# Optimization experiments

Hardware: AMD Instinct MI355X
Metric: run time of the kernel (lower is better)

## Reference

```python
import jax, jax.numpy as jnp
import numpy as np

B, T, C, H = 4, 2048, 1024, 16
D = C // H  # head_dim = 64


def setup_inputs() -> dict:
    key = jax.random.key(0)
    ks = jax.random.split(key, 5)
    scale = 0.02
    return {
        "x": jax.random.normal(ks[0], (B, T, C), dtype=jnp.float32),
        "w_qkv": jax.random.normal(ks[1], (C, 3 * C), dtype=jnp.float32) * scale,
        "b_qkv": jnp.zeros((3 * C,), dtype=jnp.float32),
        "w_out": jax.random.normal(ks[2], (C, C), dtype=jnp.float32) * scale,
        "b_out": jnp.zeros((C,), dtype=jnp.float32),
    }


def reference(x, w_qkv, b_qkv, w_out, b_out):
    Bx, Tx, Cx = x.shape
    qkv = x @ w_qkv + b_qkv  # [B,T,3C]
    q, k, v = jnp.split(qkv, 3, axis=-1)
    # [B,T,C] -> [B,H,T,D]
    def heads(t):
        return t.reshape(Bx, Tx, H, D).transpose(0, 2, 1, 3)
    q, k, v = heads(q), heads(k), heads(v)
    scores = jnp.einsum("bhtd,bhsd->bhts", q, k) / jnp.sqrt(jnp.float32(D))
    causal = jnp.tril(jnp.ones((Tx, Tx), dtype=bool))
    scores = jnp.where(causal[None, None], scores, -jnp.inf)
    attn = jax.nn.softmax(scores, axis=-1)
    y = jnp.einsum("bhts,bhsd->bhtd", attn, v)  # [B,H,T,D]
    y = y.transpose(0, 2, 1, 3).reshape(Bx, Tx, Cx)
    return y @ w_out + b_out
```

## Files before the change

### kernel.cpp

```cpp
#include <hip/hip_runtime.h>
#include <hip/hip_bf16.h>
#include <math.h>

typedef __bf16 bf16;
typedef __bf16 bf16x8 __attribute__((ext_vector_type(8)));
typedef __bf16 bf16x4 __attribute__((ext_vector_type(4)));
typedef float  f32x4  __attribute__((ext_vector_type(4)));

__device__ __forceinline__ void gld_lds16(const bf16* g, bf16* l) {
    void* gv = (void*)g;
    __builtin_amdgcn_global_load_lds(
        (__attribute__((address_space(1))) void*)gv,
        (__attribute__((address_space(3))) void*)l, 16, 0, 0);
}

__global__ void k_cvt_bf16(const float* __restrict__ in, bf16* __restrict__ out, int n4) {
    int i = blockIdx.x * blockDim.x + threadIdx.x;
    if (i < n4) {
        float4 v = ((const float4*)in)[i];
        bf16x4 o;
        o[0] = (bf16)v.x; o[1] = (bf16)v.y; o[2] = (bf16)v.z; o[3] = (bf16)v.w;
        ((bf16x4*)out)[i] = o;
    }
}

__global__ void k_transpose_cvt(const float* __restrict__ in, bf16* __restrict__ out,
                                int R, int C) {
    __shared__ float tile[64][68];
    int c0 = blockIdx.x * 64, r0 = blockIdx.y * 64;
    int tid = threadIdx.x;
#pragma unroll
    for (int i = 0; i < 4; ++i) {
        int chunk = tid + i * 256;
        int r = chunk >> 4, c4 = (chunk & 15) * 4;
        float4 v = *(const float4*)(in + (size_t)(r0 + r) * C + c0 + c4);
        tile[r][c4 + 0] = v.x; tile[r][c4 + 1] = v.y;
        tile[r][c4 + 2] = v.z; tile[r][c4 + 3] = v.w;
    }
    __syncthreads();
#pragma unroll
    for (int i = 0; i < 2; ++i) {
        int chunk = tid + i * 256;
        int c = chunk >> 3, k8 = (chunk & 7) * 8;
        bf16x8 v;
#pragma unroll
        for (int j = 0; j < 8; ++j) v[j] = (bf16)tile[k8 + j][c];
        *(bf16x8*)(out + (size_t)(c0 + c) * R + r0 + k8) = v;
    }
}

__global__ void k_transpose_v(const bf16* __restrict__ qkv, bf16* __restrict__ vt) {
    __shared__ bf16 tile[64][72];
    int bh = blockIdx.y, b = bh >> 4, h = bh & 15;
    int t0 = blockIdx.x * 64;
    int tid = threadIdx.x;
    const bf16* src = qkv + (size_t)(b * 2048 + t0) * 3072 + 2048 + h * 64;
#pragma unroll
    for (int i = 0; i < 2; ++i) {
        int chunk = tid + i * 256;
        int t = chunk >> 3, d8 = (chunk & 7) * 8;
        bf16x8 v = *(const bf16x8*)(src + (size_t)t * 3072 + d8);
#pragma unroll
        for (int j = 0; j < 8; ++j) tile[t][d8 + j] = v[j];
    }
    __syncthreads();
#pragma unroll
    for (int i = 0; i < 2; ++i) {
        int chunk = tid + i * 256;
        int d = chunk >> 3, t8 = (chunk & 7) * 8;
        bf16x8 v;
#pragma unroll
        for (int j = 0; j < 8; ++j) v[j] = tile[t8 + j][d];
        *(bf16x8*)(vt + ((size_t)bh * 64 + d) * 2048 + t0 + t8) = v;
    }
}

template <bool OUT_BF16>
__global__ __launch_bounds__(256, 2) void k_gemm(
    const bf16* __restrict__ A, const bf16* __restrict__ Bt,
    const float* __restrict__ bias, void* __restrict__ Cout,
    int M, int N, int K) {
    __shared__ __align__(16) bf16 lA[128 * 32];
    __shared__ __align__(16) bf16 lB[128 * 32];
    int tid = threadIdx.x;
    int wid = tid >> 6, lane = tid & 63;
    int quad = lane >> 4, l16 = lane & 15;
    int bm = blockIdx.y * 128, bn = blockIdx.x * 128;
    int wm = (wid >> 1) * 64, wn = (wid & 1) * 64;

    f32x4 zero = {0.f, 0.f, 0.f, 0.f};
    f32x4 acc[4][4];
#pragma unroll
    for (int i = 0; i < 4; ++i)
#pragma unroll
        for (int j = 0; j < 4; ++j) acc[i][j] = zero;

    for (int k0 = 0; k0 < K; k0 += 32) {
        __syncthreads();
#pragma unroll
        for (int i = 0; i < 2; ++i) {
            int chunk = (wid * 2 + i) * 64 + lane;
            int row = chunk >> 2, col = (chunk & 3) * 8;
            gld_lds16(A  + (size_t)(bm + row) * K + k0 + col, lA + (wid * 2 + i) * 512);
            gld_lds16(Bt + (size_t)(bn + row) * K + k0 + col, lB + (wid * 2 + i) * 512);
        }
        __syncthreads();
        bf16x8 af[4], bg[4];
#pragma unroll
        for (int i = 0; i < 4; ++i) {
            af[i] = *(const bf16x8*)(lA + (wm + i * 16 + l16) * 32 + quad * 8);
            bg[i] = *(const bf16x8*)(lB + (wn + i * 16 + l16) * 32 + quad * 8);
        }
#pragma unroll
        for (int i = 0; i < 4; ++i)
#pragma unroll
            for (int j = 0; j < 4; ++j)
                acc[i][j] = __builtin_amdgcn_mfma_f32_16x16x32_bf16(af[i], bg[j], acc[i][j], 0, 0, 0);
    }
#pragma unroll
    for (int i = 0; i < 4; ++i) {
#pragma unroll
        for (int j = 0; j < 4; ++j) {
            int col = bn + wn + j * 16 + l16;
            float bv = bias ? bias[col] : 0.f;
#pragma unroll
            for (int r = 0; r < 4; ++r) {
                int row = bm + wm + i * 16 + quad * 4 + r;
                float v = acc[i][j][r] + bv;
                if (OUT_BF16) ((bf16*)Cout)[(size_t)row * N + col] = (bf16)v;
                else          ((float*)Cout)[(size_t)row * N + col] = v;
            }
        }
    }
}

__global__ __launch_bounds__(256, 3) void k_attn(
    const bf16* __restrict__ qkv,
    const bf16* __restrict__ vt,
    bf16* __restrict__ y) {
    __shared__ __align__(16) bf16 lK[2][4096];
    __shared__ __align__(16) bf16 lV[2][4096];
    __shared__ __align__(16) bf16 lP[4][32 * 72];

    const int T = 2048, CQ = 3072;
    int tid = threadIdx.x, wid = tid >> 6, lane = tid & 63;
    int quad = lane >> 4, l16 = lane & 15;
    int x = blockIdx.x;
    int bh = ((x & 7) << 3) | ((x >> 3) & 7);
    int qb = 15 - (x >> 6);
    int b = bh >> 4, h = bh & 15;
    int q0 = qb * 128;
    int rb = qb * 4 + wid;
    int mdiag = rb >> 1;
    int ntiles = qb * 2 + 2;

    const bf16* qbase = qkv + (size_t)(b * T + q0 + wid * 32) * CQ + h * 64;
    const bf16* kbase = qkv + (size_t)(b * T) * CQ + 1024 + h * 64;
    const bf16* vbase = vt + (size_t)bh * 64 * T;
    bf16* lPw = lP[wid];

    auto stage = [&](int kt, int buf) {
        int t0 = kt * 64;
#pragma unroll
        for (int i = 0; i < 2; ++i) {
            int j = (wid * 2 + i) * 64 + lane;
            int kf = j >> 8, r = (j & 255) >> 2, c8 = (j & 3) * 8;
            gld_lds16(kbase + (size_t)(t0 + r) * CQ + kf * 32 + c8, &lK[buf][(wid * 2 + i) * 512]);
            gld_lds16(vbase + (size_t)r * T + t0 + kf * 32 + c8,    &lV[buf][(wid * 2 + i) * 512]);
        }
    };

    bf16x8 qf[2][2];
#pragma unroll
    for (int qi = 0; qi < 2; ++qi)
#pragma unroll
        for (int kf = 0; kf < 2; ++kf) {
            bf16x8 v = *(const bf16x8*)(qbase + (size_t)(qi * 16 + l16) * CQ + kf * 32 + quad * 8);
#pragma unroll
            for (int j = 0; j < 8; ++j) v[j] = (bf16)((float)v[j] * 0.125f);
            qf[qi][kf] = v;
        }

    f32x4 zero = {0.f, 0.f, 0.f, 0.f};
    f32x4 m10 = {-10.f, -10.f, -10.f, -10.f};
    f32x4 o[2][4];
    float lsum[2][4];
#pragma unroll
    for (int qi = 0; qi < 2; ++qi)
#pragma unroll
        for (int i = 0; i < 4; ++i) { o[qi][i] = zero; lsum[qi][i] = 0.f; }

    stage(0, 0);
    for (int kt = 0; kt < ntiles; ++kt) {
        __syncthreads();
        if (kt + 1 < ntiles) stage(kt + 1, (kt + 1) & 1);
        if (kt > mdiag) continue;
        const bf16* Kb = lK[kt & 1];
        const bf16* Vb = lV[kt & 1];
        bool diag = (kt == mdiag);
        bool half = diag && !(rb & 1);

        f32x4 s[2][4];
#pragma unroll
        for (int qi = 0; qi < 2; ++qi)
#pragma unroll
            for (int in = 0; in < 4; ++in) s[qi][in] = m10;
        int in_hi = half ? 2 : 4;
        for (int kf = 0; kf < 2; ++kf)
            for (int in = 0; in < in_hi; ++in) {
                bf16x8 kb = *(const bf16x8*)(Kb + kf * 2048 + (in * 16 + l16) * 32 + quad * 8);
#pragma unroll
                for (int qi = 0; qi < 2; ++qi)
                    s[qi][in] = __builtin_amdgcn_mfma_f32_16x16x32_bf16(qf[qi][kf], kb, s[qi][in], 0, 0, 0);
            }

        bf16x8 vb[2][4];
#pragma unroll
        for (int kf = 0; kf < 2; ++kf)
#pragma unroll
            for (int dn = 0; dn < 4; ++dn)
                vb[kf][dn] = *(const bf16x8*)(Vb + kf * 2048 + (dn * 16 + l16) * 32 + quad * 8);

        int rl0 = (rb * 32) - kt * 64;
        for (int qi = 0; qi < 2; ++qi)
#pragma unroll
            for (int in = 0; in < 4; ++in) {
                if (in >= in_hi) {
#pragma unroll
                    for (int r = 0; r < 4; ++r)
                        lPw[(qi * 16 + quad * 4 + r) * 72 + in * 16 + l16] = (bf16)0.f;
                    continue;
                }
#pragma unroll
                for (int r = 0; r < 4; ++r) {
                    float e = __expf(s[qi][in][r]);
                    if (diag) {
                        int col = in * 16 + l16;
                        int row = rl0 + qi * 16 + quad * 4 + r;
                        if (col > row) e = 0.f;
                    }
                    lsum[qi][r] += e;
                    lPw[(qi * 16 + quad * 4 + r) * 72 + in * 16 + l16] = (bf16)e;
                }
            }

#pragma unroll
        for (int qi = 0; qi < 2; ++qi)
#pragma unroll
            for (int kf = 0; kf < 2; ++kf) {
                bf16x8 pa = *(const bf16x8*)(lPw + (qi * 16 + l16) * 72 + kf * 32 + quad * 8);
#pragma unroll
                for (int dn = 0; dn < 4; ++dn)
                    o[qi][dn] = __builtin_amdgcn_mfma_f32_16x16x32_bf16(pa, vb[kf][dn], o[qi][dn], 0, 0, 0);
            }
    }

    float linv[2][4];
#pragma unroll
    for (int qi = 0; qi < 2; ++qi)
#pragma unroll
        for (int r = 0; r < 4; ++r) {
            float l = lsum[qi][r];
#pragma unroll
            for (int mk = 1; mk < 16; mk <<= 1) l += __shfl_xor(l, mk, 64);
            linv[qi][r] = 1.f / l;
        }
#pragma unroll
    for (int qi = 0; qi < 2; ++qi)
#pragma unroll
        for (int dn = 0; dn < 4; ++dn)
#pragma unroll
            for (int r = 0; r < 4; ++r) {
                int row = q0 + wid * 32 + qi * 16 + quad * 4 + r;
                float v = o[qi][dn][r] * linv[qi][r];
                y[(size_t)(b * T + row) * 1024 + h * 64 + dn * 16 + l16] = (bf16)v;
            }
}

extern "C" void kernel_launch(void* const* d_in, const int* in_sizes, int n_in,
                              void* d_out, int out_size, void* d_ws, size_t ws_size,
                              hipStream_t stream) {
    const float* x     = (const float*)d_in[0];
    const float* w_qkv = (const float*)d_in[1];
    const float* b_qkv = (const float*)d_in[2];
    const float* w_out = (const float*)d_in[3];
    const float* b_out = (const float*)d_in[4];
    float* out = (float*)d_out;

    const int B = 4, T = 2048, C = 1024, H = 16;
    const int M = B * T;

    char* ws = (char*)d_ws;
    bf16* xb    = (bf16*)(ws);
    bf16* wqkvT = (bf16*)(ws + (16ull << 20));
    bf16* woutT = (bf16*)(ws + (22ull << 20));
    bf16* qkvb  = (bf16*)(ws + (24ull << 20));
    bf16* yb    = (bf16*)(ws + (72ull << 20));
    bf16* vtb   = xb;

    k_cvt_bf16<<<(M * C / 4 + 255) / 256, 256, 0, stream>>>(x, xb, M * C / 4);
    k_transpose_cvt<<<dim3(3 * C / 64, C / 64), 256, 0, stream>>>(w_qkv, wqkvT, C, 3 * C);
    k_transpose_cvt<<<dim3(C / 64, C / 64), 256, 0, stream>>>(w_out, woutT, C, C);
    k_gemm<true><<<dim3(3 * C / 128, M / 128), 256, 0, stream>>>(xb, wqkvT, b_qkv, qkvb, M, 3 * C, C);
    k_transpose_v<<<dim3(T / 64, B * H), 256, 0, stream>>>(qkvb, vtb);
    k_attn<<<dim3(1024, 1), 256, 0, stream>>>(qkvb, vtb, yb);
    k_gemm<false><<<dim3(C / 128, M / 128), 256, 0, stream>>>(yb, woutT, b_out, out, M, C, C);
}
```

Measured before the change: 301.4 us.

## Deepen GEMM K-step to 64 and transpose attention score MFMA for vectorized P stores

The GEMM now stages a 64-wide K slice per iteration in two LDS halves, which halves the number of barrier pairs and loop iterations per K. In attention, the QK^T MFMA swaps its operands so each lane holds four consecutive key columns for one query row. That lets P be written to LDS as one packed bf16x4 store, and row sums become a per-lane scalar with a 2-step shuffle reduction instead of 4-step reductions over four registers. The cost is double the GEMM LDS footprint per block, which may reduce occupancy, and a changed mask and layout mapping that must stay correct.

```diff
diff --git a/kernel.cpp b/kernel.cpp
--- a/kernel.cpp
+++ b/kernel.cpp
@@ -80,8 +80,8 @@
     const bf16* __restrict__ A, const bf16* __restrict__ Bt,
     const float* __restrict__ bias, void* __restrict__ Cout,
     int M, int N, int K) {
-    __shared__ __align__(16) bf16 lA[128 * 32];
-    __shared__ __align__(16) bf16 lB[128 * 32];
+    __shared__ __align__(16) bf16 lA[2][4096];
+    __shared__ __align__(16) bf16 lB[2][4096];
     int tid = threadIdx.x;
     int wid = tid >> 6, lane = tid & 63;
     int quad = lane >> 4, l16 = lane & 15;
@@ -95,27 +95,30 @@
 #pragma unroll
         for (int j = 0; j < 4; ++j) acc[i][j] = zero;
 
-    for (int k0 = 0; k0 < K; k0 += 32) {
+    for (int k0 = 0; k0 < K; k0 += 64) {
         __syncthreads();
 #pragma unroll
-        for (int i = 0; i < 2; ++i) {
-            int chunk = (wid * 2 + i) * 64 + lane;
-            int row = chunk >> 2, col = (chunk & 3) * 8;
-            gld_lds16(A  + (size_t)(bm + row) * K + k0 + col, lA + (wid * 2 + i) * 512);
-            gld_lds16(Bt + (size_t)(bn + row) * K + k0 + col, lB + (wid * 2 + i) * 512);
+        for (int i = 0; i < 4; ++i) {
+            int j = (wid * 4 + i) * 64 + lane;
+            int kf = j >> 9, row = (j & 511) >> 2, c8 = (j & 3) * 8;
+            gld_lds16(A  + (size_t)(bm + row) * K + k0 + kf * 32 + c8, &lA[0][0] + (wid * 4 + i) * 512);
+            gld_lds16(Bt + (size_t)(bn + row) * K + k0 + kf * 32 + c8, &lB[0][0] + (wid * 4 + i) * 512);
         }
         __syncthreads();
-        bf16x8 af[4], bg[4];
-#pragma unroll
-        for (int i = 0; i < 4; ++i) {
-            af[i] = *(const bf16x8*)(lA + (wm + i * 16 + l16) * 32 + quad * 8);
-            bg[i] = *(const bf16x8*)(lB + (wn + i * 16 + l16) * 32 + quad * 8);
-        }
-#pragma unroll
-        for (int i = 0; i < 4; ++i)
-#pragma unroll
-            for (int j = 0; j < 4; ++j)
-                acc[i][j] = __builtin_amdgcn_mfma_f32_16x16x32_bf16(af[i], bg[j], acc[i][j], 0, 0, 0);
+#pragma unroll
+        for (int kk = 0; kk < 2; ++kk) {
+            bf16x8 af[4], bg[4];
+#pragma unroll
+            for (int i = 0; i < 4; ++i) {
+                af[i] = *(const bf16x8*)(&lA[kk][(wm + i * 16 + l16) * 32 + quad * 8]);
+                bg[i] = *(const bf16x8*)(&lB[kk][(wn + i * 16 + l16) * 32 + quad * 8]);
+            }
+#pragma unroll
+            for (int i = 0; i < 4; ++i)
+#pragma unroll
+                for (int j = 0; j < 4; ++j)
+                    acc[i][j] = __builtin_amdgcn_mfma_f32_16x16x32_bf16(af[i], bg[j], acc[i][j], 0, 0, 0);
+        }
     }
 #pragma unroll
     for (int i = 0; i < 4; ++i) {
@@ -184,11 +187,11 @@
     f32x4 zero = {0.f, 0.f, 0.f, 0.f};
     f32x4 m10 = {-10.f, -10.f, -10.f, -10.f};
     f32x4 o[2][4];
-    float lsum[2][4];
+    float lsum[2] = {0.f, 0.f};
 #pragma unroll
     for (int qi = 0; qi < 2; ++qi)
 #pragma unroll
-        for (int i = 0; i < 4; ++i) { o[qi][i] = zero; lsum[qi][i] = 0.f; }
+        for (int i = 0; i < 4; ++i) o[qi][i] = zero;
 
     stage(0, 0);
     for (int kt = 0; kt < ntiles; ++kt) {
@@ -199,19 +202,19 @@
         const bf16* Vb = lV[kt & 1];
         bool diag = (kt == mdiag);
         bool half = diag && !(rb & 1);
+        int in_hi = half ? 2 : 4;
 
         f32x4 s[2][4];
 #pragma unroll
         for (int qi = 0; qi < 2; ++qi)
 #pragma unroll
             for (int in = 0; in < 4; ++in) s[qi][in] = m10;
-        int in_hi = half ? 2 : 4;
         for (int kf = 0; kf < 2; ++kf)
             for (int in = 0; in < in_hi; ++in) {
                 bf16x8 kb = *(const bf16x8*)(Kb + kf * 2048 + (in * 16 + l16) * 32 + quad * 8);
 #pragma unroll
                 for (int qi = 0; qi < 2; ++qi)
-                    s[qi][in] = __builtin_amdgcn_mfma_f32_16x16x32_bf16(qf[qi][kf], kb, s[qi][in], 0, 0, 0);
+                    s[qi][in] = __builtin_amdgcn_mfma_f32_16x16x32_bf16(kb, qf[qi][kf], s[qi][in], 0, 0, 0);
             }
 
         bf16x8 vb[2][4];
@@ -222,27 +225,28 @@
                 vb[kf][dn] = *(const bf16x8*)(Vb + kf * 2048 + (dn * 16 + l16) * 32 + quad * 8);
 
         int rl0 = (rb * 32) - kt * 64;
-        for (int qi = 0; qi < 2; ++qi)
+        for (int qi = 0; qi < 2; ++qi) {
+            int qloc = rl0 + qi * 16 + l16;
 #pragma unroll
             for (int in = 0; in < 4; ++in) {
+                bf16x4 pk4;
                 if (in >= in_hi) {
-#pragma unroll
-                    for (int r = 0; r < 4; ++r)
-                        lPw[(qi * 16 + quad * 4 + r) * 72 + in * 16 + l16] = (bf16)0.f;
-                    continue;
+                    pk4[0] = pk4[1] = pk4[2] = pk4[3] = (bf16)0.f;
+                } else {
+#pragma unroll
+                    for (int r = 0; r < 4; ++r) {
+                        float e = __expf(s[qi][in][r]);
+                        if (diag) {
+                            int tloc = in * 16 + quad * 4 + r;
+                            if (tloc > qloc) e = 0.f;
+                        }
+                        lsum[qi] += e;
+                        pk4[r] = (bf16)e;
+                    }
                 }
-#pragma unroll
-                for (int r = 0; r < 4; ++r) {
-                    float e = __expf(s[qi][in][r]);
-                    if (diag) {
-                        int col = in * 16 + l16;
-                        int row = rl0 + qi * 16 + quad * 4 + r;
-                        if (col > row) e = 0.f;
-                    }
-                    lsum[qi][r] += e;
-                    lPw[(qi * 16 + quad * 4 + r) * 72 + in * 16 + l16] = (bf16)e;
-                }
-            }
+                *(bf16x4*)(lPw + (qi * 16 + l16) * 72 + in * 16 + quad * 4) = pk4;
+            }
+        }
 
 #pragma unroll
         for (int qi = 0; qi < 2; ++qi)
@@ -255,26 +259,26 @@
             }
     }
 
-    float linv[2][4];
+    float linv[2];
+#pragma unroll
+    for (int qi = 0; qi < 2; ++qi) {
+        float l = lsum[qi];
+        l += __shfl_xor(l, 16, 64);
+        l += __shfl_xor(l, 32, 64);
+        linv[qi] = 1.f / l;
+    }
 #pragma unroll
     for (int qi = 0; qi < 2; ++qi)
 #pragma unroll
         for (int r = 0; r < 4; ++r) {
-            float l = lsum[qi][r];
-#pragma unroll
-            for (int mk = 1; mk < 16; mk <<= 1) l += __shfl_xor(l, mk, 64);
-            linv[qi][r] = 1.f / l;
-        }
-#pragma unroll
-    for (int qi = 0; qi < 2; ++qi)
-#pragma unroll
-        for (int dn = 0; dn < 4; ++dn)
-#pragma unroll
-            for (int r = 0; r < 4; ++r) {
-                int row = q0 + wid * 32 + qi * 16 + quad * 4 + r;
-                float v = o[qi][dn][r] * linv[qi][r];
+            float li = __shfl(linv[qi], quad * 4 + r, 64);
+            int row = q0 + wid * 32 + qi * 16 + quad * 4 + r;
+#pragma unroll
+            for (int dn = 0; dn < 4; ++dn) {
+                float v = o[qi][dn][r] * li;
                 y[(size_t)(b * T + row) * 1024 + h * 64 + dn * 16 + l16] = (bf16)v;
             }
+        }
 }
 
 extern "C" void kernel_launch(void* const* d_in, const int* in_sizes, int n_in,
```

Measured after the change: 281.1 us. 6.7% less time.
